# Performance work log

Hardware: AMD Instinct MI355X
Metric: run time of the kernel (lower is better)

## Reference

```python
import jax, jax.numpy as jnp
import numpy as np
from jax import lax

STRIDE = 1
PAD = 1


def setup_inputs() -> dict:
    key = jax.random.key(0)
    ks = jax.random.split(key, 6)
    B, C, H, W = 32, 256, 56, 56
    E, O, K = 4, 256, 3
    HID = max(C // 4, 8)  # 64
    return {
        "x": jax.random.normal(ks[0], (B, C, H, W), dtype=jnp.float32),
        "experts": jax.random.normal(ks[1], (E, O, C, K, K), dtype=jnp.float32),
        "rw1": jax.random.normal(ks[2], (HID, C), dtype=jnp.float32) * 0.05,
        "rb1": jax.random.normal(ks[3], (HID,), dtype=jnp.float32) * 0.05,
        "rw2": jax.random.normal(ks[4], (E, HID), dtype=jnp.float32) * 0.05,
        "rb2": jax.random.normal(ks[5], (E,), dtype=jnp.float32) * 0.05,
    }


def reference(x, experts, rw1, rb1, rw2, rb2):
    B, C, H, W = x.shape
    E, O, _, K, _ = experts.shape
    # Routing: global avg pool -> 1x1 conv (matmul) -> relu -> 1x1 conv -> softmax
    pooled = x.mean(axis=(2, 3))                      # [B, C]
    h = jax.nn.relu(pooled @ rw1.T + rb1)             # [B, HID]
    routing = jax.nn.softmax(h @ rw2.T + rb2, axis=-1)  # [B, E]
    # Per-sample mixed conv weights: [B, O, C, K, K]
    combined = jnp.einsum('be,eocij->bocij', routing, experts)
    # Per-sample conv as a single grouped conv: groups = B
    x_g = x.reshape(1, B * C, H, W)
    w_g = combined.reshape(B * O, C, K, K)
    out = lax.conv_general_dilated(
        x_g, w_g,
        window_strides=(STRIDE, STRIDE),
        padding=[(PAD, PAD), (PAD, PAD)],
        dimension_numbers=('NCHW', 'OIHW', 'NCHW'),
        feature_group_count=B,
    )  # [1, B*O, H', W']
    Ho, Wo = out.shape[2], out.shape[3]
    return out.reshape(B, O, Ho, Wo)
```

## Files before the change

### kernel.cpp

```cpp
#include <hip/hip_runtime.h>


#define B_  32
#define C_  256
#define H_  56
#define W_  56
#define HW_ 3136
#define E_  4
#define O_  256
#define HID_ 64
#define HP_ 58
#define PHW_ 3364
#define KK_ 2304

typedef __attribute__((ext_vector_type(8))) short bf16x8;
typedef __attribute__((ext_vector_type(4))) float f32x4;

__device__ __forceinline__ unsigned short f2bf(float f) {
    unsigned int u = __float_as_uint(f);
    u = (u + 0x7FFFu + ((u >> 16) & 1u)) >> 16;
    return (unsigned short)u;
}

__device__ __forceinline__ unsigned int cvt_pk_bf16(float lo, float hi) {
    unsigned int r;
    asm("v_cvt_pk_bf16_f32 %0, %1, %2" : "=v"(r) : "v"(lo), "v"(hi));
    return r;
}

__device__ __forceinline__ void load_lds16(const void* g, void* l) {
    __builtin_amdgcn_global_load_lds(
        (__attribute__((address_space(1))) unsigned int*)(unsigned long long)(const char*)g,
        (__attribute__((address_space(3))) unsigned int*)l,
        16, 0, 0);
}

__device__ __forceinline__ void wgbar() {
    asm volatile("" ::: "memory");
    __builtin_amdgcn_s_barrier();
    asm volatile("" ::: "memory");
}

#define VMW(N) asm volatile("s_waitcnt vmcnt(" #N ")" ::: "memory")

__global__ __launch_bounds__(256) void transform_pool(const float* __restrict__ x,
                                                      unsigned short* __restrict__ xp,
                                                      float* __restrict__ pp) {
    const int h    = blockIdx.x;
    const int half = blockIdx.y;
    const int b    = blockIdx.z;
    const int t    = threadIdx.x;
    const int c0   = half * 128;
    __shared__ alignas(16) float tile[128 * 64];
    __shared__ alignas(16) float part[14 * 128];

    const float* src = x + ((size_t)(b * C_ + c0) * H_ + h) * W_;
#pragma unroll
    for (int i = t; i < 128 * 14; i += 256) {
        const int c  = i / 14;
        const int w4 = (i % 14) * 4;
        float4 v = *(const float4*)(src + (size_t)c * (H_ * W_) + w4);
        const int wsw = w4 ^ (((c >> 3) & 7) << 2);
        *(float4*)&tile[c * 64 + wsw] = v;
    }

    unsigned int* ubase = (unsigned int*)(xp + (size_t)b * PHW_ * C_);
    {
        const int hp = h + 1;
        if (t < 128) {
            const int col = (t >> 6) ? 57 : 0;
            const int cu  = t & 63;
            ubase[((size_t)hp * HP_ + col) * 128 + half * 64 + cu] = 0u;
        }
        if (h == 0) {
            for (int i = t; i < HP_ * 64; i += 256) {
                const int pix = i >> 6, cu = i & 63;
                ubase[(size_t)pix * 128 + half * 64 + cu] = 0u;
                ubase[((size_t)57 * HP_ + pix) * 128 + half * 64 + cu] = 0u;
            }
        }
    }
    __syncthreads();

    const int cu  = t & 15;
    const int seg = t >> 4;
    float s0 = 0.f, s1 = 0.f, s2 = 0.f, s3 = 0.f;
    float s4 = 0.f, s5 = 0.f, s6 = 0.f, s7 = 0.f;
    if (seg < 14) {
        const int sw = (cu & 7) << 2;
        unsigned short* ob = xp
            + ((size_t)(b * HP_ + h + 1) * HP_ + (seg * 4 + 1)) * C_ + c0 + cu * 8;
#pragma unroll
        for (int wi = 0; wi < 4; ++wi) {
            const int wc = (seg * 4 + wi) ^ sw;
            const float* tp = tile + cu * 512 + wc;
            float f0 = tp[0 * 64], f1 = tp[1 * 64], f2 = tp[2 * 64], f3 = tp[3 * 64];
            float f4 = tp[4 * 64], f5 = tp[5 * 64], f6 = tp[6 * 64], f7 = tp[7 * 64];
            s0 += f0; s1 += f1; s2 += f2; s3 += f3;
            s4 += f4; s5 += f5; s6 += f6; s7 += f7;
            uint4 pk;
            pk.x = cvt_pk_bf16(f0, f1);
            pk.y = cvt_pk_bf16(f2, f3);
            pk.z = cvt_pk_bf16(f4, f5);
            pk.w = cvt_pk_bf16(f6, f7);
            *(uint4*)(ob + (size_t)wi * C_) = pk;
        }
        *(float4*)&part[seg * 128 + cu * 8 + 0] = make_float4(s0, s1, s2, s3);
        *(float4*)&part[seg * 128 + cu * 8 + 4] = make_float4(s4, s5, s6, s7);
    }
    __syncthreads();
    if (t < 128) {
        float v = 0.f;
#pragma unroll
        for (int sgi = 0; sgi < 14; ++sgi) v += part[sgi * 128 + t];
        pp[((size_t)(b * C_ + c0 + t)) * 56 + h] = v;
    }
}

__global__ void routing_kernel(const float* __restrict__ pp,
                               const float* __restrict__ rw1,
                               const float* __restrict__ rb1,
                               const float* __restrict__ rw2,
                               const float* __restrict__ rb2,
                               float* __restrict__ routing) {
    const int b = blockIdx.x;
    const int t = threadIdx.x;
    __shared__ float pl[C_];
    __shared__ float part[256];
    __shared__ float hb[HID_];
    __shared__ float lg[E_];
    {
        const float* p = pp + (size_t)(b * C_ + t) * 56;
        float s = 0.f;
#pragma unroll
        for (int i = 0; i < 14; ++i) {
            float4 v = *(const float4*)(p + 4 * i);
            s += v.x + v.y + v.z + v.w;
        }
        pl[t] = s * (1.0f / (float)HW_);
    }
    __syncthreads();
    const int j = t >> 2, seg = t & 3;
    {
        const float* w = rw1 + j * C_ + seg * 64;
        const float* p = pl + seg * 64;
        float s = 0.0f;
#pragma unroll 8
        for (int cc = 0; cc < 64; ++cc) s += p[cc] * w[cc];
        part[t] = s;
    }
    __syncthreads();
    if (seg == 0) {
        float s = part[t] + part[t + 1] + part[t + 2] + part[t + 3] + rb1[j];
        hb[j] = fmaxf(s, 0.0f);
    }
    __syncthreads();
    if (t < E_) {
        float s = rb2[t];
        for (int jj = 0; jj < HID_; ++jj) s += hb[jj] * rw2[t * HID_ + jj];
        lg[t] = s;
    }
    __syncthreads();
    if (t == 0) {
        float mx = fmaxf(fmaxf(lg[0], lg[1]), fmaxf(lg[2], lg[3]));
        float e0 = expf(lg[0] - mx), e1 = expf(lg[1] - mx);
        float e2 = expf(lg[2] - mx), e3 = expf(lg[3] - mx);
        float inv = 1.0f / (e0 + e1 + e2 + e3);
        routing[b * E_ + 0] = e0 * inv;
        routing[b * E_ + 1] = e1 * inv;
        routing[b * E_ + 2] = e2 * inv;
        routing[b * E_ + 3] = e3 * inv;
    }
}

__global__ void combine_kernel(const float* __restrict__ experts,
                               const float* __restrict__ routing,
                               unsigned short* __restrict__ wcomb) {
    const int o  = blockIdx.x;
    const int bg = blockIdx.y;
    const int c  = threadIdx.x;
    __shared__ alignas(16) unsigned short sh[KK_];
    __shared__ float rt[16];
    if (c < 16) rt[c] = routing[bg * 16 + c];

    float w[E_][9];
#pragma unroll
    for (int e = 0; e < E_; ++e) {
        const float* ep = experts + ((size_t)(e * O_ + o) * C_ + c) * 9;
        float4 v0 = *(const float4*)(ep + 0);
        float4 v1 = *(const float4*)(ep + 4);
        w[e][0] = v0.x; w[e][1] = v0.y; w[e][2] = v0.z; w[e][3] = v0.w;
        w[e][4] = v1.x; w[e][5] = v1.y; w[e][6] = v1.z; w[e][7] = v1.w;
        w[e][8] = ep[8];
    }
    __syncthreads();
#pragma unroll
    for (int bq = 0; bq < 4; ++bq) {
        const float r0 = rt[bq * 4 + 0], r1 = rt[bq * 4 + 1];
        const float r2 = rt[bq * 4 + 2], r3 = rt[bq * 4 + 3];
#pragma unroll
        for (int k = 0; k < 9; ++k) {
            float a = r0 * w[0][k] + r1 * w[1][k] + r2 * w[2][k] + r3 * w[3][k];
            sh[k * C_ + c] = f2bf(a);
        }
        __syncthreads();
        const int b = bg * 4 + bq;
        uint4* dst = (uint4*)(wcomb + (size_t)(b * O_ + o) * KK_);
        const uint4* s4 = (const uint4*)sh;
        for (int idx = c; idx < KK_ / 8; idx += 256) dst[idx] = s4[idx];
        __syncthreads();
    }
}

__global__ __launch_bounds__(512) void conv_gemm(const unsigned short* __restrict__ xp,
                                                 const unsigned short* __restrict__ wcomb,
                                                 float* __restrict__ out) {
    __shared__ alignas(16) unsigned short Alds[2 * 2 * 128 * 64];
    __shared__ alignas(16) unsigned short Blds[2 * 2 * 128 * 64];

    const int tid  = threadIdx.x;
    const int lane = tid & 63;
    const int wid  = tid >> 6;
    const int wm   = wid >> 2;
    const int wn   = wid & 3;
    const int fm   = lane & 15;
    const int fq   = lane >> 4;

    const int id  = blockIdx.x;
    const int xcd = id & 7;
    const int qq  = id >> 3;
    const int b   = (qq / 13) * 8 + xcd;
    const int n0  = (qq % 13) * 256;

    const int rl = wid * 8 + (lane >> 3);
    const int qg = (lane & 7) ^ ((lane >> 3) & 7);
    const unsigned short* abase = wcomb + ((size_t)b * O_ + rl) * KK_ + qg * 8;
    const unsigned short* bbase = xp + (size_t)b * PHW_ * C_ + qg * 8;
    unsigned int boffs[2][2];
#pragma unroll
    for (int u = 0; u < 2; ++u)
#pragma unroll
        for (int s = 0; s < 2; ++s) {
            int pi = (u * 2 + (rl >> 5)) * 64 + s * 32 + (rl & 31);
            int p  = n0 + pi;
            if (p > HW_ - 1) p = HW_ - 1;
            boffs[u][s] = (unsigned int)((p / W_) * HP_ + (p % W_)) * C_;
        }

#define STAGE_A(BUF, S, KT)                                                     \
    {                                                                           \
        const unsigned short* asrc_ = abase + (size_t)((S) * 64) * KK_ + (KT) * 64; \
        load_lds16(asrc_,                    Alds + (((BUF) * 2 + (S)) * 128 + wid * 8) * 64);      \
        load_lds16(asrc_ + (size_t)128 * KK_, Alds + (((BUF) * 2 + (S)) * 128 + 64 + wid * 8) * 64); \
    }

#define STAGE_B(BUF, S, KT)                                                     \
    {                                                                           \
        const int r9_  = (KT) >> 2;                                             \
        const int duB_ = ((r9_ / 3) * HP_ + (r9_ % 3)) * C_ + ((KT) & 3) * 64;  \
        load_lds16(bbase + boffs[0][S] + duB_, Blds + (((BUF) * 2 + (S)) * 128 + wid * 8) * 64);      \
        load_lds16(bbase + boffs[1][S] + duB_, Blds + (((BUF) * 2 + (S)) * 128 + 64 + wid * 8) * 64); \
    }

    f32x4 acc[8][4];
#pragma unroll
    for (int i = 0; i < 8; ++i)
#pragma unroll
        for (int j = 0; j < 4; ++j) acc[i][j] = (f32x4){0.f, 0.f, 0.f, 0.f};
    bf16x8 af[4][2];

    const int colk0 = ((0 + fq) ^ (fm & 7)) * 8;
    const int colk1 = ((4 + fq) ^ (fm & 7)) * 8;
    const int arow  = (wm * 64 + fm) * 64;
    const int brow  = (wn * 32 + fm) * 64;

#define PHASE(MH, NH, BUF, WCODE, STAGE_STMT, RDAF)                             \
    {                                                                           \
        WCODE;                                                                  \
        wgbar();                                                                \
        if (RDAF) {                                                             \
            _Pragma("unroll")                                                   \
            for (int q_ = 0; q_ < 4; ++q_) {                                    \
                af[q_][0] = *(const bf16x8*)(Alds + (((BUF) * 2 + (MH)) * 128) * 64 + arow + q_ * 1024 + colk0); \
                af[q_][1] = *(const bf16x8*)(Alds + (((BUF) * 2 + (MH)) * 128) * 64 + arow + q_ * 1024 + colk1); \
            }                                                                   \
        }                                                                       \
        bf16x8 bv[2][2];                                                        \
        _Pragma("unroll")                                                       \
        for (int j_ = 0; j_ < 2; ++j_) {                                        \
            bv[j_][0] = *(const bf16x8*)(Blds + (((BUF) * 2 + (NH)) * 128) * 64 + brow + j_ * 1024 + colk0); \
            bv[j_][1] = *(const bf16x8*)(Blds + (((BUF) * 2 + (NH)) * 128) * 64 + brow + j_ * 1024 + colk1); \
        }                                                                       \
        STAGE_STMT;                                                             \
        asm volatile("" ::: "memory");                                          \
        __builtin_amdgcn_s_setprio(1);                                          \
        _Pragma("unroll")                                                       \
        for (int q_ = 0; q_ < 4; ++q_)                                          \
            _Pragma("unroll")                                                   \
            for (int j_ = 0; j_ < 2; ++j_) {                                    \
                acc[(MH) * 4 + q_][(NH) * 2 + j_] = __builtin_amdgcn_mfma_f32_16x16x32_bf16( \
                    af[q_][0], bv[j_][0], acc[(MH) * 4 + q_][(NH) * 2 + j_], 0, 0, 0);       \
                acc[(MH) * 4 + q_][(NH) * 2 + j_] = __builtin_amdgcn_mfma_f32_16x16x32_bf16( \
                    af[q_][1], bv[j_][1], acc[(MH) * 4 + q_][(NH) * 2 + j_], 0, 0, 0);       \
            }                                                                   \
        __builtin_amdgcn_s_setprio(0);                                          \
    }

    STAGE_A(0, 0, 0); STAGE_B(0, 0, 0); STAGE_A(0, 1, 0); STAGE_B(0, 1, 0);
    STAGE_A(1, 0, 1); STAGE_B(1, 0, 1);

#pragma unroll 1
    for (int i = 0; i < 17; ++i) {
        const int k2 = 2 * i;
        PHASE(0, 0, 0, VMW(8),  STAGE_A(1, 1, k2 + 1), 1)
        PHASE(0, 1, 0, VMW(6),  STAGE_B(1, 1, k2 + 1), 0)
        PHASE(1, 0, 0, VMW(10), STAGE_A(0, 0, k2 + 2), 1)
        PHASE(1, 1, 0,        , STAGE_B(0, 0, k2 + 2), 0)
        PHASE(0, 0, 1, VMW(8),  STAGE_A(0, 1, k2 + 2), 1)
        PHASE(0, 1, 1, VMW(6),  STAGE_B(0, 1, k2 + 2), 0)
        PHASE(1, 0, 1, VMW(10), STAGE_A(1, 0, k2 + 3), 1)
        PHASE(1, 1, 1,        , STAGE_B(1, 0, k2 + 3), 0)
    }
    PHASE(0, 0, 0, VMW(8),  STAGE_A(1, 1, 35), 1)
    PHASE(0, 1, 0, VMW(6),  STAGE_B(1, 1, 35), 0)
    PHASE(1, 0, 0, VMW(10), (void)0, 1)
    PHASE(1, 1, 0,        , (void)0, 0)
    PHASE(0, 0, 1, VMW(4),  (void)0, 1)
    PHASE(0, 1, 1, VMW(0),  (void)0, 0)
    PHASE(1, 0, 1, VMW(0),  (void)0, 1)
    PHASE(1, 1, 1,        , (void)0, 0)

#pragma unroll
    for (int mi = 0; mi < 8; ++mi) {
        const int o = wm * 128 + mi * 16 + fq * 4;
#pragma unroll
        for (int ni = 0; ni < 4; ++ni) {
            const int p = n0 + wn * 64 + ni * 16 + fm;
            if (p < HW_) {
                float* po = out + ((size_t)(b * O_ + o)) * HW_ + p;
                po[0 * HW_] = acc[mi][ni][0];
                po[1 * HW_] = acc[mi][ni][1];
                po[2 * (size_t)HW_] = acc[mi][ni][2];
                po[3 * (size_t)HW_] = acc[mi][ni][3];
            }
        }
    }
#undef PHASE
#undef STAGE_A
#undef STAGE_B
}

extern "C" void kernel_launch(void* const* d_in, const int* in_sizes, int n_in,
                              void* d_out, int out_size, void* d_ws, size_t ws_size,
                              hipStream_t stream) {
    const float* x       = (const float*)d_in[0];
    const float* experts = (const float*)d_in[1];
    const float* rw1     = (const float*)d_in[2];
    const float* rb1     = (const float*)d_in[3];
    const float* rw2     = (const float*)d_in[4];
    const float* rb2     = (const float*)d_in[5];
    float* out = (float*)d_out;

    const size_t XP_OFF = 0;
    const size_t WC_OFF = 55115776;
    const size_t PP_OFF = WC_OFF + 37748736;
    const size_t RT_OFF = PP_OFF + 1835008;
    unsigned short* xp    = (unsigned short*)((char*)d_ws + XP_OFF);
    unsigned short* wcomb = (unsigned short*)((char*)d_ws + WC_OFF);
    float* pp      = (float*)((char*)d_ws + PP_OFF);
    float* routing = (float*)((char*)d_ws + RT_OFF);

    transform_pool<<<dim3(H_, 2, B_), dim3(256), 0, stream>>>(x, xp, pp);
    routing_kernel<<<dim3(B_), dim3(256), 0, stream>>>(pp, rw1, rb1, rw2, rb2, routing);
    combine_kernel<<<dim3(O_, 8), dim3(256), 0, stream>>>(experts, routing, wcomb);
    conv_gemm<<<dim3(416), dim3(512), 0, stream>>>(xp, wcomb, out);
}
```

Measured before the change: 346.6 us.

## Restructure GEMM main loop into ping-pong tile phases with explicit LDS waits

Replaces the per-phase GEMM loop with a DO_TILE macro that splits each k-tile into four MFMA quadrants. Each quadrant keeps separate A/B fragment registers (afA/afB, bv0/bv1) so LDS reads can be reused across quadrants. It adds explicit lgkmcnt waits, sched_barriers, and barriers both before and after each MFMA block, and reorders global-to-LDS staging so A(1,1) is prefetched in the prologue. The aim is tighter control over overlap between LDS reads, global loads and MFMA issue. The cost is more workgroup barriers and higher register pressure from the duplicated fragment buffers.

```diff
diff --git a/kernel.cpp b/kernel.cpp
--- a/kernel.cpp
+++ b/kernel.cpp
@@ -42,6 +42,7 @@
 }
 
 #define VMW(N) asm volatile("s_waitcnt vmcnt(" #N ")" ::: "memory")
+#define LGKM(N) asm volatile("s_waitcnt lgkmcnt(" #N ")" ::: "memory")
 
 __global__ __launch_bounds__(256) void transform_pool(const float* __restrict__ x,
                                                       unsigned short* __restrict__ xp,
@@ -250,7 +251,7 @@
 #define STAGE_A(BUF, S, KT)                                                     \
     {                                                                           \
         const unsigned short* asrc_ = abase + (size_t)((S) * 64) * KK_ + (KT) * 64; \
-        load_lds16(asrc_,                    Alds + (((BUF) * 2 + (S)) * 128 + wid * 8) * 64);      \
+        load_lds16(asrc_,                     Alds + (((BUF) * 2 + (S)) * 128 + wid * 8) * 64);      \
         load_lds16(asrc_ + (size_t)128 * KK_, Alds + (((BUF) * 2 + (S)) * 128 + 64 + wid * 8) * 64); \
     }
 
@@ -267,68 +268,103 @@
     for (int i = 0; i < 8; ++i)
 #pragma unroll
         for (int j = 0; j < 4; ++j) acc[i][j] = (f32x4){0.f, 0.f, 0.f, 0.f};
-    bf16x8 af[4][2];
 
     const int colk0 = ((0 + fq) ^ (fm & 7)) * 8;
     const int colk1 = ((4 + fq) ^ (fm & 7)) * 8;
     const int arow  = (wm * 64 + fm) * 64;
     const int brow  = (wn * 32 + fm) * 64;
 
-#define PHASE(MH, NH, BUF, WCODE, STAGE_STMT, RDAF)                             \
-    {                                                                           \
-        WCODE;                                                                  \
-        wgbar();                                                                \
-        if (RDAF) {                                                             \
-            _Pragma("unroll")                                                   \
-            for (int q_ = 0; q_ < 4; ++q_) {                                    \
-                af[q_][0] = *(const bf16x8*)(Alds + (((BUF) * 2 + (MH)) * 128) * 64 + arow + q_ * 1024 + colk0); \
-                af[q_][1] = *(const bf16x8*)(Alds + (((BUF) * 2 + (MH)) * 128) * 64 + arow + q_ * 1024 + colk1); \
-            }                                                                   \
-        }                                                                       \
-        bf16x8 bv[2][2];                                                        \
+    bf16x8 afA[4][2], afB[4][2], bv0[2][2], bv1[2][2];
+
+#define RD_AF(DST, BUF, MH)                                                     \
+    _Pragma("unroll")                                                           \
+    for (int q_ = 0; q_ < 4; ++q_) {                                            \
+        const unsigned short* ap_ = Alds + (((BUF) * 2 + (MH)) * 128) * 64 + arow + q_ * 1024; \
+        DST[q_][0] = *(const bf16x8*)(ap_ + colk0);                             \
+        DST[q_][1] = *(const bf16x8*)(ap_ + colk1);                             \
+    }
+
+#define RD_BV(DST, BUF, NH)                                                     \
+    _Pragma("unroll")                                                           \
+    for (int j_ = 0; j_ < 2; ++j_) {                                            \
+        const unsigned short* bp_ = Blds + (((BUF) * 2 + (NH)) * 128) * 64 + brow + j_ * 1024; \
+        DST[j_][0] = *(const bf16x8*)(bp_ + colk0);                             \
+        DST[j_][1] = *(const bf16x8*)(bp_ + colk1);                             \
+    }
+
+#define MFMA_Q(MH, NH, AF, BV)                                                  \
+    __builtin_amdgcn_s_setprio(1);                                              \
+    _Pragma("unroll")                                                           \
+    for (int q_ = 0; q_ < 4; ++q_)                                              \
         _Pragma("unroll")                                                       \
         for (int j_ = 0; j_ < 2; ++j_) {                                        \
-            bv[j_][0] = *(const bf16x8*)(Blds + (((BUF) * 2 + (NH)) * 128) * 64 + brow + j_ * 1024 + colk0); \
-            bv[j_][1] = *(const bf16x8*)(Blds + (((BUF) * 2 + (NH)) * 128) * 64 + brow + j_ * 1024 + colk1); \
+            acc[(MH) * 4 + q_][(NH) * 2 + j_] = __builtin_amdgcn_mfma_f32_16x16x32_bf16( \
+                AF[q_][0], BV[j_][0], acc[(MH) * 4 + q_][(NH) * 2 + j_], 0, 0, 0);       \
+            acc[(MH) * 4 + q_][(NH) * 2 + j_] = __builtin_amdgcn_mfma_f32_16x16x32_bf16( \
+                AF[q_][1], BV[j_][1], acc[(MH) * 4 + q_][(NH) * 2 + j_], 0, 0, 0);       \
         }                                                                       \
-        STAGE_STMT;                                                             \
-        asm volatile("" ::: "memory");                                          \
-        __builtin_amdgcn_s_setprio(1);                                          \
-        _Pragma("unroll")                                                       \
-        for (int q_ = 0; q_ < 4; ++q_)                                          \
-            _Pragma("unroll")                                                   \
-            for (int j_ = 0; j_ < 2; ++j_) {                                    \
-                acc[(MH) * 4 + q_][(NH) * 2 + j_] = __builtin_amdgcn_mfma_f32_16x16x32_bf16( \
-                    af[q_][0], bv[j_][0], acc[(MH) * 4 + q_][(NH) * 2 + j_], 0, 0, 0);       \
-                acc[(MH) * 4 + q_][(NH) * 2 + j_] = __builtin_amdgcn_mfma_f32_16x16x32_bf16( \
-                    af[q_][1], bv[j_][1], acc[(MH) * 4 + q_][(NH) * 2 + j_], 0, 0, 0);       \
-            }                                                                   \
-        __builtin_amdgcn_s_setprio(0);                                          \
+    __builtin_amdgcn_s_setprio(0);
+
+#define DO_TILE(BUF, S1, S2, S3, S4, W4)                                        \
+    {                                                                           \
+                                                             \
+        RD_AF(afA, BUF, 0)                                                      \
+        RD_BV(bv0, BUF, 0)                                                      \
+        S1;                                                                     \
+        LGKM(8);                                                                \
+        wgbar();                                                                \
+        LGKM(0);                                                                \
+        __builtin_amdgcn_sched_barrier(0);                                      \
+        MFMA_Q(0, 0, afA, bv0)                                                  \
+        wgbar();                                                                \
+                                                             \
+        RD_BV(bv1, BUF, 1)                                                      \
+        S2;                                                                     \
+        wgbar();                                                                \
+        LGKM(0);                                                                \
+        __builtin_amdgcn_sched_barrier(0);                                      \
+        MFMA_Q(0, 1, afA, bv1)                                                  \
+        wgbar();                                                                \
+                                                             \
+        RD_AF(afB, BUF, 1)                                                      \
+        S3;                                                                     \
+        wgbar();                                                                \
+        LGKM(0);                                                                \
+        __builtin_amdgcn_sched_barrier(0);                                      \
+        MFMA_Q(1, 0, afB, bv0)                                                  \
+        wgbar();                                                                \
+                                                             \
+        S4;                                                                     \
+        W4;                                                                     \
+        wgbar();                                                                \
+        __builtin_amdgcn_sched_barrier(0);                                      \
+        MFMA_Q(1, 1, afB, bv1)                                                  \
+        wgbar();                                                                \
     }
 
     STAGE_A(0, 0, 0); STAGE_B(0, 0, 0); STAGE_A(0, 1, 0); STAGE_B(0, 1, 0);
-    STAGE_A(1, 0, 1); STAGE_B(1, 0, 1);
+    STAGE_A(1, 0, 1); STAGE_B(1, 0, 1); STAGE_A(1, 1, 1);
+    VMW(6);
+    wgbar();
 
 #pragma unroll 1
     for (int i = 0; i < 17; ++i) {
         const int k2 = 2 * i;
-        PHASE(0, 0, 0, VMW(8),  STAGE_A(1, 1, k2 + 1), 1)
-        PHASE(0, 1, 0, VMW(6),  STAGE_B(1, 1, k2 + 1), 0)
-        PHASE(1, 0, 0, VMW(10), STAGE_A(0, 0, k2 + 2), 1)
-        PHASE(1, 1, 0,        , STAGE_B(0, 0, k2 + 2), 0)
-        PHASE(0, 0, 1, VMW(8),  STAGE_A(0, 1, k2 + 2), 1)
-        PHASE(0, 1, 1, VMW(6),  STAGE_B(0, 1, k2 + 2), 0)
-        PHASE(1, 0, 1, VMW(10), STAGE_A(1, 0, k2 + 3), 1)
-        PHASE(1, 1, 1,        , STAGE_B(1, 0, k2 + 3), 0)
-    }
-    PHASE(0, 0, 0, VMW(8),  STAGE_A(1, 1, 35), 1)
-    PHASE(0, 1, 0, VMW(6),  STAGE_B(1, 1, 35), 0)
-    PHASE(1, 0, 0, VMW(10), (void)0, 1)
-    PHASE(1, 1, 0,        , (void)0, 0)
-    PHASE(0, 0, 1, VMW(4),  (void)0, 1)
-    PHASE(0, 1, 1, VMW(0),  (void)0, 0)
-    PHASE(1, 0, 1, VMW(0),  (void)0, 1)
-    PHASE(1, 1, 1,        , (void)0, 0)
+        DO_TILE(0,
+                STAGE_B(1, 1, k2 + 1),
+                STAGE_A(0, 0, k2 + 2),
+                STAGE_B(0, 0, k2 + 2),
+                STAGE_A(0, 1, k2 + 2),
+                VMW(6))
+        DO_TILE(1,
+                STAGE_B(0, 1, k2 + 2),
+                STAGE_A(1, 0, k2 + 3),
+                STAGE_B(1, 0, k2 + 3),
+                STAGE_A(1, 1, k2 + 3),
+                VMW(6))
+    }
+    DO_TILE(0, STAGE_B(1, 1, 35), (void)0, (void)0, (void)0, VMW(0))
+    DO_TILE(1, (void)0, (void)0, (void)0, (void)0, (void)0)
 
 #pragma unroll
     for (int mi = 0; mi < 8; ++mi) {
@@ -345,7 +381,10 @@
             }
         }
     }
-#undef PHASE
+#undef DO_TILE
+#undef MFMA_Q
+#undef RD_AF
+#undef RD_BV
 #undef STAGE_A
 #undef STAGE_B
 }
```

Result: faster. 337.3 us (-2.7%).
